# Performance work log

Hardware: AMD Instinct MI355X
Metric: run time of the kernel (lower is better)

The kernel has to match this reference:

```python
import jax, jax.numpy as jnp
import numpy as np
from jax.scipy.special import logsumexp

_INF = 1e10
_GAMMA_MIN = 1e-4

ALPHA_SHAPE, ALPHA_TEMPORAL, ALPHA_BOUNDARY, ALPHA_ORDER, ALPHA_COVERAGE = 0.3, 0.2, 0.2, 0.15, 0.15
GAMMA = 0.1


def _softmin3(a, b, c, g):
    return -g * logsumexp(jnp.stack([-a, -b, -c]) / g, axis=0)


def _soft_dtw_alignment(cost, gamma):
    """Anti-diagonal wavefront soft-DTW fwd+bwd; returns (alignment (M,N), distance).
    Diagonals are carried as length-(m+1)/(m+2) buffers indexed directly by i,
    so carry size is O(m) per scan step (vjp-friendly)."""
    m, n = cost.shape
    g = max(gamma, _GAMMA_MIN)

    ii = jnp.arange(m + 1)

    def fwd_step(carry, d):
        Dm1, Dm2 = carry  # diagonals d-1, d-2: buf[i] = R[i, d'-i]
        jj = d - ii
        valid = (ii >= 1) & (ii <= m) & (jj >= 1) & (jj <= n)
        im1 = jnp.maximum(ii - 1, 0)
        sm = _softmin3(Dm2[im1], Dm1[im1], Dm1[ii], g)  # diag, above, left
        ci = jnp.clip(ii - 1, 0, m - 1)
        cj = jnp.clip(jj - 1, 0, n - 1)
        Dnew = jnp.where(valid, cost[ci, cj] + sm, _INF)
        return (Dnew, Dm1), Dnew

    D0 = jnp.full((m + 1,), _INF, cost.dtype).at[0].set(0.0)  # R[0,0] = 0
    D1 = jnp.full((m + 1,), _INF, cost.dtype)
    _, fdiags = jax.lax.scan(fwd_step, (D1, D0), jnp.arange(2, m + n + 1))
    # fdiags[t, i] = R[i, (t+2)-i]
    I = jnp.arange(1, m + 1)[:, None]
    J = jnp.arange(1, n + 1)[None, :]
    f_vals = fdiags[I + J - 2, I]  # R_fwd[1:m+1, 1:n+1]
    distance = fdiags[m + n - 2, m]  # R_fwd[m, n]

    kk = jnp.arange(m + 2)

    def bwd_step(carry, d):
        Ep1, Ep2 = carry  # diagonals d+1, d+2 of R_bwd
        jj = d - kk
        valid = (kk >= 1) & (kk <= m) & (jj >= 1) & (jj <= n)
        ip1 = jnp.minimum(kk + 1, m + 1)
        ci = jnp.clip(kk, 0, m - 1)
        cim = jnp.clip(kk - 1, 0, m - 1)
        cj = jnp.clip(jj, 0, n - 1)
        cjm = jnp.clip(jj - 1, 0, n - 1)
        diag_c = jnp.where((kk + 1 <= m) & (jj + 1 <= n), Ep2[ip1] + cost[ci, cj], _INF)
        below_c = jnp.where(kk + 1 <= m, Ep1[ip1] + cost[ci, cjm], _INF)
        right_c = jnp.where(jj + 1 <= n, Ep1[kk] + cost[cim, cj], _INF)
        Enew = jnp.where(valid, _softmin3(diag_c, below_c, right_c, g), _INF)
        return (Enew, Ep1), Enew

    Ebase = jnp.full((m + 2,), _INF, cost.dtype).at[m].set(0.0)  # R_bwd[m,n]=0 (diag m+n)
    Etop = jnp.full((m + 2,), _INF, cost.dtype)
    _, bdiags = jax.lax.scan(bwd_step, (Ebase, Etop), jnp.arange(m + n - 1, 0, -1))
    # bdiags row t <-> d = m+n-1-t ; b_vals[i-1, j-1] = R_bwd[i, j]
    d_ij = I + J
    row = jnp.clip(m + n - 1 - d_ij, 0, m + n - 2)
    b_vals = jnp.where(d_ij == m + n, 0.0, bdiags[row, I])

    log_prob = jnp.minimum(-(f_vals + cost + b_vals - distance) / g, 0.0)
    alignment = jnp.exp(log_prob)
    total = alignment.sum()
    scale = jnp.where(total > 1e-8, float(min(m, n)) / jnp.maximum(total, 1e-8), 1.0)
    return alignment * scale, distance


def sop_dilate_loss(pred, target, gb):
    M, N = target.shape[0], pred.shape[0]
    # squared euclidean pairwise cost (M, N)
    t2 = jnp.sum(target * target, axis=-1)[:, None]
    p2 = jnp.sum(pred * pred, axis=-1)[None, :]
    cost = jnp.maximum(t2 + p2 - 2.0 * (target @ pred.T), 0.0)

    alignment, shape_loss = _soft_dtw_alignment(cost, GAMMA)

    i_pos = jnp.arange(M, dtype=cost.dtype) / max(M - 1, 1)
    j_pos = jnp.arange(N, dtype=cost.dtype) / max(N - 1, 1)
    temporal = jnp.sum(alignment * (i_pos[:, None] - j_pos[None, :]) ** 2)

    internal = [b for b in gb if 0 < b < M]
    if internal:
        bi = jnp.array(internal)
        dev = (j_pos[None, :] - (bi[:, None].astype(cost.dtype) / max(M - 1, 1))) ** 2
        boundary = jnp.sum(alignment[bi] * dev) / len(internal)
    else:
        boundary = jnp.asarray(0.0, cost.dtype)

    order = jnp.asarray(0.0, cost.dtype)
    if len(gb) > 2:
        pos = []
        for s in range(len(gb) - 1):
            st, en = gb[s], gb[s + 1]
            if st >= M or en > M or st >= en:
                continue
            colsum = alignment[st:en].sum(axis=0)
            mass = jnp.maximum(colsum.sum(), 1e-8)
            pos.append(jnp.sum(colsum * j_pos) / mass)
        for k in range(1, len(pos)):
            order = order + jax.nn.relu(pos[k - 1] - pos[k])
        if len(pos) > 1:
            order = order / (len(pos) - 1)

    coverage = jnp.asarray(0.0, cost.dtype)
    n_steps = len(gb) - 1
    if n_steps > 0:
        for s in range(n_steps):
            st, en = gb[s], min(gb[s + 1], M)
            if st >= en:
                continue
            coverage = coverage + jax.nn.relu((en - st) * 0.5 - alignment[st:en].sum())
        coverage = coverage / n_steps

    total = (ALPHA_SHAPE * shape_loss + ALPHA_TEMPORAL * temporal
             + ALPHA_BOUNDARY * boundary + ALPHA_ORDER * order
             + ALPHA_COVERAGE * coverage)
    return total


def setup_inputs() -> dict:
    key = jax.random.key(0)
    k1, k2 = jax.random.split(key)
    T1, T2, D = 2048, 2048, 64  # pred len, target len, feature dim
    pred = jax.random.normal(k1, (T1, D), dtype=jnp.float32)
    target = jax.random.normal(k2, (T2, D), dtype=jnp.float32)
    gold_boundaries = (jnp.arange(9, dtype=jnp.int32) * 256)  # [0,256,...,2048]
    return {"pred": pred, "target": target, "gold_boundaries": gold_boundaries}


def reference(pred, target, gold_boundaries):
    gb = [int(v) for v in np.asarray(gold_boundaries)]
    return sop_dilate_loss(pred, target, gb)
```

## Files before the change

### kernel.cpp

```cpp
#include <hip/hip_runtime.h>

#define MM 2048
#define NN 2048
#define DD 64
#define NDIAG (MM + NN - 1)
#define TOTCELLS (MM * NN)
#define MAXSEG 15

#define NWGD   4
#define NWAVE  4
#define STRIPROWS 128
#define TPS    32
#define BT     16
#define NSUPER 152
#define GRING  1024
#define LRING  256

constexpr float K2      = 14.426950408889634f;
constexpr float INF_K   = 1.0e10f * 14.426950408889634f;
constexpr float UNSCALE = 0.06931471805599453f;

__device__ __forceinline__ int diag_off(int d) {
    return (d < NN) ? ((d * (d + 1)) >> 1)
                    : (TOTCELLS - (((NDIAG - d) * (NDIAG - d + 1)) >> 1));
}
__device__ __forceinline__ int diag_imin(int d) { return (d < NN) ? 0 : (d - (NN - 1)); }
__device__ __forceinline__ int diag_len(int d)  { return (d < NN) ? (d + 1) : (NDIAG - d); }

__device__ __forceinline__ float fexp2(float x) { return __builtin_amdgcn_exp2f(x); }
__device__ __forceinline__ float flog2(float x) { return __builtin_amdgcn_logf(x); }

__device__ __forceinline__ float rot_up1(float x) {
    int xi = __builtin_bit_cast(int, x);
    int r  = __builtin_amdgcn_update_dpp(xi, xi, 0x13C, 0xF, 0xF, true);
    return __builtin_bit_cast(float, r);
}

__device__ __forceinline__ float softmin3k(float a, float b, float c) {
    const float m1 = fminf(fminf(a, b), c);
    const float m2 = __builtin_amdgcn_fmed3f(a, b, c);
    const float m3 = fmaxf(fmaxf(a, b), c);
    const float e  = 1.0f + fexp2(m1 - m2) + fexp2(m1 - m3);
    return m1 - flog2(e);
}

__global__ __launch_bounds__(256) void cost_kernel(const float* __restrict__ pred,
                                                   const float* __restrict__ target,
                                                   float* __restrict__ costD,
                                                   float* __restrict__ acc) {
    __shared__ float Ts[64][65];
    __shared__ float Ps[64][65];
    const int tid = threadIdx.x;
    const int tx = tid & 15, ty = tid >> 4;
    const int i0 = blockIdx.y * 64;
    const int j0 = blockIdx.x * 64;

    if (blockIdx.x == 0 && blockIdx.y == 0 && tid < 80) ((unsigned*)acc)[tid] = 0u;

    #pragma unroll
    for (int rnd = 0; rnd < 4; ++rnd) {
        int f4i = tid + rnd * 256;
        int r  = f4i >> 4;
        int k4 = (f4i & 15) << 2;
        float4 tv = *reinterpret_cast<const float4*>(target + (size_t)(i0 + r) * DD + k4);
        Ts[r][k4 + 0] = tv.x; Ts[r][k4 + 1] = tv.y; Ts[r][k4 + 2] = tv.z; Ts[r][k4 + 3] = tv.w;
        float4 pv = *reinterpret_cast<const float4*>(pred + (size_t)(j0 + r) * DD + k4);
        Ps[k4 + 0][r] = pv.x; Ps[k4 + 1][r] = pv.y; Ps[k4 + 2][r] = pv.z; Ps[k4 + 3][r] = pv.w;
    }
    __syncthreads();

    float accv[4][4];
    #pragma unroll
    for (int a = 0; a < 4; ++a)
        #pragma unroll
        for (int b = 0; b < 4; ++b) accv[a][b] = 0.f;

    for (int k = 0; k < 64; ++k) {
        float ta[4], pb[4];
        #pragma unroll
        for (int a = 0; a < 4; ++a) ta[a] = Ts[ty + 16 * a][k];
        #pragma unroll
        for (int b = 0; b < 4; ++b) pb[b] = Ps[k][tx + 16 * b];
        #pragma unroll
        for (int a = 0; a < 4; ++a)
            #pragma unroll
            for (int b = 0; b < 4; ++b) {
                float d = ta[a] - pb[b];
                accv[a][b] = fmaf(d, d, accv[a][b]);
            }
    }
    #pragma unroll
    for (int a = 0; a < 4; ++a) {
        int i = i0 + ty + 16 * a;
        #pragma unroll
        for (int b = 0; b < 4; ++b) {
            int j = j0 + tx + 16 * b;
            int d = i + j;
            costD[diag_off(d) + (i - diag_imin(d))] = accv[a][b] * K2;
        }
    }
}

__global__ __launch_bounds__(256) void dp_pipe(const float* __restrict__ costD,
                                               float* __restrict__ fwdD,
                                               float* __restrict__ bwdR,
                                               unsigned* __restrict__ flagsP,
                                               float* __restrict__ gringP) {
    __shared__ float cls[2][NWAVE][TPS][STRIPROWS];
    __shared__ float ring[NWAVE + 1][LRING];
    const int dir  = (int)blockIdx.x >> 2;
    const int wg   = (int)blockIdx.x & 3;
    const int tid  = threadIdx.x;
    const int wv   = tid >> 6;
    const int lane = tid & 63;
    const int g    = wg * NWAVE + wv;
    const int gu   = __builtin_amdgcn_readfirstlane(g);
    const int Og   = __builtin_amdgcn_readfirstlane(32 * g + 96 * (g >> 2));
    const int Suse = __builtin_amdgcn_readfirstlane(160 * g + 96 * (g >> 2));
    const int r0   = STRIPROWS * g + 2 * lane;
    float* __restrict__ outD = dir ? bwdR : fwdD;
    unsigned* pf = flagsP + dir * NWGD;
    float* grd   = gringP + (size_t)dir * 3 * GRING;
    const float* mring = ring[(wv == 0) ? NWAVE : (wv - 1)];
    const int lam4 = (lane & 31) << 2;
    const int lamS = dir ? -lam4 : lam4;
    const int eoff = dir ? ((2 * lane) ^ 2) : (2 * lane);

    int aS = r0;

    auto STAGE = [&](int tb, int bsel) {
        #pragma unroll
        for (int k = 0; k < 16; ++k) {
            const int dd0 = tb + 2 * k - Og;
            const int dc0 = (dd0 < 0) ? 0 : ((dd0 > NDIAG - 1) ? NDIAG - 1 : dd0);
            int b0 = diag_off(dc0) - diag_imin(dc0) + STRIPROWS * gu;
            const int dd1 = dd0 + 1;
            const int dc1 = (dd1 < 0) ? 0 : ((dd1 > NDIAG - 1) ? NDIAG - 1 : dd1);
            int b1 = diag_off(dc1) - diag_imin(dc1) + STRIPROWS * gu;
            if (dir) { b0 = TOTCELLS - 4 - b0; b1 = TOTCELLS - 4 - b1; }
            int src = ((lane < 32) ? b0 : b1) + lamS;
            src = (src < 0) ? 0 : ((src > TOTCELLS - 4) ? (TOTCELLS - 4) : src);
            __builtin_amdgcn_global_load_lds(
                (const __attribute__((address_space(1))) void*)(costD + src),
                (__attribute__((address_space(3))) void*)&cls[bsel][wv][2 * k][0],
                16, 0, 0);
        }
    };

    float Rk0 = INF_K, Rk0m1 = INF_K, Rk1 = INF_K;
    float dg0 = (g == 0 && lane == 0) ? 0.0f : INF_K;

    STAGE(0, 0);
    __syncthreads();

    for (unsigned m = 0; m < NSUPER; ++m) {
        const int T0 = (int)(m * TPS);
        const int bsel = (int)(m & 1);

        if (wv == 0 && wg > 0) {
            const int c0g = T0 - Suse;
            if (c0g + 63 >= 0 && c0g < NN) {
                const unsigned need = (m >= 3) ? (m - 3) : 0;
                unsigned guard = 0;
                while (__hip_atomic_load(&pf[wg - 1], __ATOMIC_ACQUIRE,
                                         __HIP_MEMORY_SCOPE_AGENT) < need &&
                       guard < (1u << 20)) { __builtin_amdgcn_s_sleep(8); ++guard; }
                const int c = c0g + lane;
                if (c >= 0 && c < NN)
                    ring[NWAVE][c & (LRING - 1)] =
                        __hip_atomic_load(&grd[(wg - 1) * GRING + (c & (GRING - 1))],
                                          __ATOMIC_RELAXED, __HIP_MEMORY_SCOPE_AGENT);
            }
        }

        if (m + 1 < NSUPER) STAGE(T0 + TPS, bsel ^ 1);

        #pragma unroll
        for (int h = 0; h < 2; ++h) {
            const int B0 = T0 + h * BT;
            float2 cb[BT];
            float  eb[BT];
            if (dir) {
                #pragma unroll
                for (int p = 0; p < BT; ++p) {
                    float2 r = *reinterpret_cast<const float2*>(
                        &cls[bsel][wv][h * BT + p][eoff]);
                    cb[p].x = r.y; cb[p].y = r.x;
                }
            } else {
                #pragma unroll
                for (int p = 0; p < BT; ++p)
                    cb[p] = *reinterpret_cast<const float2*>(
                        &cls[bsel][wv][h * BT + p][eoff]);
            }
            if (g != 0) {
                #pragma unroll
                for (int p = 0; p < BT; ++p)
                    eb[p] = mring[((unsigned)(B0 + p - Suse)) & (LRING - 1)];
            } else {
                #pragma unroll
                for (int p = 0; p < BT; ++p) eb[p] = INF_K;
            }

            #pragma unroll
            for (int p = 0; p < BT; ++p) {
                const int t  = B0 + p;
                const int dd = t - Og;
                if (dd >= 0 && dd < NDIAG) {
                    const int ec = t - Suse;
                    float extv = INF_K;
                    if (g != 0 && ec >= 0 && ec < NN) extv = eb[p];
                    const float shr = rot_up1(Rk1);
                    const float up0 = (lane == 0) ? extv : shr;
                    const float n0 = cb[p].x + softmin3k(dg0, up0, Rk0);
                    const float n1 = cb[p].y + softmin3k(Rk0m1, Rk0, Rk1);
                    const int c0 = dd - r0;
                    const bool v0 = (c0 >= 0) && (c0 < NN);
                    const bool v1 = (c0 >= 1) && (c0 <= NN);
                    Rk0m1 = Rk0;
                    if (v0) Rk0 = n0;
                    if (v1) Rk1 = n1;
                    dg0 = up0;
                    if (v0) outD[aS] = Rk0;
                    if (v1) outD[aS + 1] = Rk1;
                    const int pc = ec - (STRIPROWS - 1);
                    if (lane == 63 && pc >= 0 && pc < NN)
                        ring[wv][pc & (LRING - 1)] = Rk1;
                    const int ds = (dd + 1 < NDIAG - 1 - dd) ? (dd + 1) : (NDIAG - 1 - dd);
                    aS += ds;
                }
            }
        }
        __syncthreads();

        if (wv == 0 && wg < NWGD - 1) {
            const int Sp = 736 * wg + 480;
            const int cb0 = T0 - Sp - (STRIPROWS - 1);
            if (lane < TPS) {
                const int c = cb0 + lane;
                if (c >= 0 && c < NN)
                    __hip_atomic_store(&grd[wg * GRING + (c & (GRING - 1))],
                                       ring[NWAVE - 1][c & (LRING - 1)],
                                       __ATOMIC_RELAXED, __HIP_MEMORY_SCOPE_AGENT);
            }
            if (lane == 0)
                __hip_atomic_store(&pf[wg], m + 1, __ATOMIC_RELEASE,
                                   __HIP_MEMORY_SCOPE_AGENT);
        }
    }
}

__device__ __forceinline__ float wave_red(float v) {
    v += __shfl_xor(v, 32, 64);
    v += __shfl_xor(v, 16, 64);
    v += __shfl_xor(v, 8, 64);
    v += __shfl_xor(v, 4, 64);
    v += __shfl_xor(v, 2, 64);
    v += __shfl_xor(v, 1, 64);
    return v;
}

__global__ __launch_bounds__(256) void combine_kernel(const float* __restrict__ fwdD,
                                                      const float* __restrict__ bwdR,
                                                      const int* __restrict__ gbp, int ngb,
                                                      float* __restrict__ acc) {
    const int d = blockIdx.x;
    const int ofs = diag_off(d), imin = diag_imin(d), len = diag_len(d);
    const float dist = fwdD[TOTCELLS - 1];
    __shared__ float sseg[MAXSEG], ssegp[MAXSEG];
    __shared__ int sgb[MAXSEG + 1];
    const int tid = threadIdx.x;
    if (tid < MAXSEG) { sseg[tid] = 0.f; ssegp[tid] = 0.f; }
    if (tid < ngb && tid <= MAXSEG) sgb[tid] = gbp[tid];
    __syncthreads();

    float pT = 0.f, pTe = 0.f, pB = 0.f;
    const float invM1 = 1.f / (float)(MM - 1);
    const float invN1 = 1.f / (float)(NN - 1);
    const int nseg = ngb - 1;

    for (int x = tid; x < len; x += 256) {
        const int i0 = imin + x, j0 = d - i0;
        const float f = fwdD[ofs + x];
        const float b = bwdR[TOTCELLS - 1 - (ofs + x)];
        const float a = fexp2(-fmaxf(f + b - dist, 0.0f));
        const float jp = j0 * invN1, ip = i0 * invM1;
        pT += a;
        const float dt = ip - jp;
        pTe += a * dt * dt;
        int s = -1;
        for (int q = 0; q < nseg && q < MAXSEG; ++q)
            if (i0 >= sgb[q] && i0 < sgb[q + 1]) s = q;
        if (s >= 0) { atomicAdd(&sseg[s], a); atomicAdd(&ssegp[s], a * jp); }
        for (int q = 0; q < ngb && q <= MAXSEG; ++q) {
            const int bv = sgb[q];
            if (bv > 0 && bv < MM && i0 == bv) {
                const float dv = jp - (float)bv * invM1;
                pB += a * dv * dv;
            }
        }
    }
    pT = wave_red(pT); pTe = wave_red(pTe); pB = wave_red(pB);
    if ((tid & 63) == 0) {
        if (pT  != 0.f) atomicAdd(&acc[0], pT);
        if (pTe != 0.f) atomicAdd(&acc[1], pTe);
        if (pB  != 0.f) atomicAdd(&acc[2], pB);
    }
    __syncthreads();
    if (tid < nseg && tid < MAXSEG) {
        if (sseg[tid]  != 0.f) atomicAdd(&acc[3 + tid], sseg[tid]);
        if (ssegp[tid] != 0.f) atomicAdd(&acc[3 + MAXSEG + tid], ssegp[tid]);
    }
}

__global__ void final_kernel(const float* __restrict__ acc,
                             const float* __restrict__ fwdD,
                             const int* __restrict__ gbp, int ngb,
                             float* __restrict__ out) {
    if (threadIdx.x != 0 || blockIdx.x != 0) return;
    const float dist = fwdD[TOTCELLS - 1] * UNSCALE;
    const float Utot = acc[0];
    const float scale = (Utot > 1e-8f) ? ((float)(MM < NN ? MM : NN) / fmaxf(Utot, 1e-8f)) : 1.0f;
    const float temporal = scale * acc[1];

    int gb[MAXSEG + 1];
    const int n = (ngb <= MAXSEG + 1) ? ngb : (MAXSEG + 1);
    for (int q = 0; q < n; ++q) gb[q] = gbp[q];

    int nint = 0;
    for (int q = 0; q < n; ++q) if (gb[q] > 0 && gb[q] < MM) nint++;
    const float boundary = (nint > 0) ? (scale * acc[2] / (float)nint) : 0.f;

    float order = 0.f;
    if (n > 2) {
        float pos[MAXSEG];
        int np = 0;
        for (int s = 0; s + 1 < n; ++s) {
            const int st = gb[s], en = gb[s + 1];
            if (st >= MM || en > MM || st >= en) continue;
            const float mass = fmaxf(scale * acc[3 + s], 1e-8f);
            pos[np++] = scale * acc[3 + MAXSEG + s] / mass;
        }
        for (int k = 1; k < np; ++k) order += fmaxf(pos[k - 1] - pos[k], 0.f);
        if (np > 1) order /= (float)(np - 1);
    }

    float cov = 0.f;
    const int nsteps = n - 1;
    if (nsteps > 0) {
        for (int s = 0; s < nsteps; ++s) {
            const int st = gb[s];
            int en = gb[s + 1]; if (en > MM) en = MM;
            if (st >= en) continue;
            cov += fmaxf((float)(en - st) * 0.5f - scale * acc[3 + s], 0.f);
        }
        cov /= (float)nsteps;
    }

    out[0] = 0.3f * dist + 0.2f * temporal + 0.2f * boundary + 0.15f * order + 0.15f * cov;
}

extern "C" void kernel_launch(void* const* d_in, const int* in_sizes, int n_in,
                              void* d_out, int out_size, void* d_ws, size_t ws_size,
                              hipStream_t stream) {
    const float* pred   = (const float*)d_in[0];
    const float* target = (const float*)d_in[1];
    const int*   gb     = (const int*)d_in[2];
    const int ngb = in_sizes[2];

    float* costD = (float*)d_ws;
    float* fwdD  = costD + TOTCELLS;
    float* bwdR  = fwdD + TOTCELLS;
    float* acc   = bwdR + TOTCELLS;
    unsigned* flagsP = (unsigned*)(acc + 64);
    float* gringP    = (float*)(flagsP + 2 * NWGD);

    cost_kernel<<<dim3(NN / 64, MM / 64), 256, 0, stream>>>(pred, target, costD, acc);
    dp_pipe<<<2 * NWGD, NWAVE * 64, 0, stream>>>(costD, fwdD, bwdR, flagsP, gringP);
    combine_kernel<<<NDIAG, 256, 0, stream>>>(fwdD, bwdR, gb, ngb, acc);
    final_kernel<<<1, 64, 0, stream>>>(acc, fwdD, gb, ngb, (float*)d_out);
}
```

Before: 1.453 ms.

## Add branch-free interior fast path, relax barrier waitcnt, and LUT segment lookup

The wavefront DP kernel gains a fast path for 16-step blocks lying fully inside the strip, which drops the per-step validity predicates and masked stores. It also skips blocks that fall entirely outside the diagonal range. The per-superstep __syncthreads is replaced by a manual s_waitcnt that leaves up to 48 vector-memory ops in flight before s_barrier, so prefetch loads can overlap the barrier. The combine kernel precomputes per-row segment and boundary lookup tables in shared memory instead of looping over boundaries for every cell, at the cost of an extra table build per block and reliance on hand-tuned waitcnt counts that could be wrong.

```diff
diff --git a/kernel.cpp b/kernel.cpp
--- a/kernel.cpp
+++ b/kernel.cpp
@@ -122,6 +122,9 @@
     unsigned* pf = flagsP + dir * NWGD;
     float* grd   = gringP + (size_t)dir * 3 * GRING;
     const float* mring = ring[(wv == 0) ? NWAVE : (wv - 1)];
+    const bool l0  = (lane == 0);
+    const bool l63 = (lane == 63);
+    const bool useExt = (g != 0);
     const int lam4 = (lane & 31) << 2;
     const int lamS = dir ? -lam4 : lam4;
     const int eoff = dir ? ((2 * lane) ^ 2) : (2 * lane);
@@ -174,10 +177,17 @@
         }
 
         if (m + 1 < NSUPER) STAGE(T0 + TPS, bsel ^ 1);
+        __builtin_amdgcn_sched_barrier(0);
+
+        const bool fullS = (T0 - Og >= 0) && (T0 + TPS - 1 - Og <= NDIAG - 1);
+        const int glo = STRIPROWS * gu;
 
         #pragma unroll
         for (int h = 0; h < 2; ++h) {
             const int B0 = T0 + h * BT;
+            const int ddlo = B0 - Og, ddhi = B0 + BT - 1 - Og;
+            if (ddhi < 0 || ddlo >= NDIAG) continue;
+
             float2 cb[BT];
             float  eb[BT];
             if (dir) {
@@ -193,7 +203,7 @@
                     cb[p] = *reinterpret_cast<const float2*>(
                         &cls[bsel][wv][h * BT + p][eoff]);
             }
-            if (g != 0) {
+            if (useExt) {
                 #pragma unroll
                 for (int p = 0; p < BT; ++p)
                     eb[p] = mring[((unsigned)(B0 + p - Suse)) & (LRING - 1)];
@@ -202,36 +212,60 @@
                 for (int p = 0; p < BT; ++p) eb[p] = INF_K;
             }
 
-            #pragma unroll
-            for (int p = 0; p < BT; ++p) {
-                const int t  = B0 + p;
-                const int dd = t - Og;
-                if (dd >= 0 && dd < NDIAG) {
-                    const int ec = t - Suse;
-                    float extv = INF_K;
-                    if (g != 0 && ec >= 0 && ec < NN) extv = eb[p];
+            const bool fast = (ddlo >= glo + STRIPROWS) && (ddhi <= glo + NN - 1);
+            if (fast) {
+                #pragma unroll
+                for (int p = 0; p < BT; ++p) {
+                    const int t  = B0 + p;
+                    const int dd = t - Og;
                     const float shr = rot_up1(Rk1);
-                    const float up0 = (lane == 0) ? extv : shr;
+                    const float up0 = l0 ? eb[p] : shr;
                     const float n0 = cb[p].x + softmin3k(dg0, up0, Rk0);
                     const float n1 = cb[p].y + softmin3k(Rk0m1, Rk0, Rk1);
-                    const int c0 = dd - r0;
-                    const bool v0 = (c0 >= 0) && (c0 < NN);
-                    const bool v1 = (c0 >= 1) && (c0 <= NN);
-                    Rk0m1 = Rk0;
-                    if (v0) Rk0 = n0;
-                    if (v1) Rk1 = n1;
-                    dg0 = up0;
-                    if (v0) outD[aS] = Rk0;
-                    if (v1) outD[aS + 1] = Rk1;
-                    const int pc = ec - (STRIPROWS - 1);
-                    if (lane == 63 && pc >= 0 && pc < NN)
-                        ring[wv][pc & (LRING - 1)] = Rk1;
-                    const int ds = (dd + 1 < NDIAG - 1 - dd) ? (dd + 1) : (NDIAG - 1 - dd);
-                    aS += ds;
+                    Rk0m1 = Rk0; Rk0 = n0; Rk1 = n1; dg0 = up0;
+                    outD[aS] = n0;
+                    outD[aS + 1] = n1;
+                    if (l63) ring[wv][(t - Suse - (STRIPROWS - 1)) & (LRING - 1)] = n1;
+                    aS += (dd + 1 < NDIAG - 1 - dd) ? (dd + 1) : (NDIAG - 1 - dd);
                 }
-            }
-        }
-        __syncthreads();
+            } else {
+                #pragma unroll
+                for (int p = 0; p < BT; ++p) {
+                    const int t  = B0 + p;
+                    const int dd = t - Og;
+                    if (dd >= 0 && dd < NDIAG) {
+                        const int ec = t - Suse;
+                        float extv = INF_K;
+                        if (useExt && ec >= 0 && ec < NN) extv = eb[p];
+                        const float shr = rot_up1(Rk1);
+                        const float up0 = l0 ? extv : shr;
+                        const float n0 = cb[p].x + softmin3k(dg0, up0, Rk0);
+                        const float n1 = cb[p].y + softmin3k(Rk0m1, Rk0, Rk1);
+                        const int c0 = dd - r0;
+                        const bool v0 = (c0 >= 0) && (c0 < NN);
+                        const bool v1 = (c0 >= 1) && (c0 <= NN);
+                        Rk0m1 = Rk0;
+                        if (v0) Rk0 = n0;
+                        if (v1) Rk1 = n1;
+                        dg0 = up0;
+                        if (v0) outD[aS] = Rk0;
+                        if (v1) outD[aS + 1] = Rk1;
+                        const int pc = ec - (STRIPROWS - 1);
+                        if (l63 && pc >= 0 && pc < NN)
+                            ring[wv][pc & (LRING - 1)] = Rk1;
+                        aS += (dd + 1 < NDIAG - 1 - dd) ? (dd + 1) : (NDIAG - 1 - dd);
+                    }
+                }
+            }
+        }
+
+        if (fullS) {
+            asm volatile("s_waitcnt vmcnt(48) lgkmcnt(0)" ::: "memory");
+        } else {
+            asm volatile("s_waitcnt vmcnt(0) lgkmcnt(0)" ::: "memory");
+        }
+        __builtin_amdgcn_sched_barrier(0);
+        __builtin_amdgcn_s_barrier();
 
         if (wv == 0 && wg < NWGD - 1) {
             const int Sp = 736 * wg + 480;
@@ -269,15 +303,29 @@
     const float dist = fwdD[TOTCELLS - 1];
     __shared__ float sseg[MAXSEG], ssegp[MAXSEG];
     __shared__ int sgb[MAXSEG + 1];
+    __shared__ signed char slut[MM];
+    __shared__ signed char bflag[MM];
     const int tid = threadIdx.x;
     if (tid < MAXSEG) { sseg[tid] = 0.f; ssegp[tid] = 0.f; }
     if (tid < ngb && tid <= MAXSEG) sgb[tid] = gbp[tid];
     __syncthreads();
 
+    const int nseg = ngb - 1;
+    for (int r = tid; r < MM; r += 256) {
+        int sres = -1;
+        for (int q = 0; q < nseg && q < MAXSEG; ++q)
+            if (r >= sgb[q] && r < sgb[q + 1]) sres = q;
+        slut[r] = (signed char)sres;
+        int bf = 0;
+        for (int q = 0; q < ngb && q <= MAXSEG; ++q)
+            if (sgb[q] == r && r > 0 && r < MM) bf = 1;
+        bflag[r] = (signed char)bf;
+    }
+    __syncthreads();
+
     float pT = 0.f, pTe = 0.f, pB = 0.f;
     const float invM1 = 1.f / (float)(MM - 1);
     const float invN1 = 1.f / (float)(NN - 1);
-    const int nseg = ngb - 1;
 
     for (int x = tid; x < len; x += 256) {
         const int i0 = imin + x, j0 = d - i0;
@@ -288,16 +336,11 @@
         pT += a;
         const float dt = ip - jp;
         pTe += a * dt * dt;
-        int s = -1;
-        for (int q = 0; q < nseg && q < MAXSEG; ++q)
-            if (i0 >= sgb[q] && i0 < sgb[q + 1]) s = q;
+        const int s = slut[i0];
         if (s >= 0) { atomicAdd(&sseg[s], a); atomicAdd(&ssegp[s], a * jp); }
-        for (int q = 0; q < ngb && q <= MAXSEG; ++q) {
-            const int bv = sgb[q];
-            if (bv > 0 && bv < MM && i0 == bv) {
-                const float dv = jp - (float)bv * invM1;
-                pB += a * dv * dv;
-            }
+        if (bflag[i0]) {
+            const float dv = jp - (float)i0 * invM1;
+            pB += a * dv * dv;
         }
     }
     pT = wave_red(pT); pTe = wave_red(pTe); pB = wave_red(pB);
```

Measured after the change: 1.343 ms. -7.5%, faster.
